# Optimization experiments

Hardware: AMD Instinct MI355X
Metric: run time of the kernel (lower is better)

## Reference

```python
import jax, jax.numpy as jnp
import numpy as np


def setup_inputs() -> dict:
    key = jax.random.key(0)
    k1, k2, k3, k4, k5 = jax.random.split(key, 5)
    B, D, T = 32, 256, 32       # batch, word_feature_dim, seq_len
    Dh, H, Wd = 128, 128, 128   # image_feature_dim, height, width
    word_features = jax.random.normal(k1, (B, D, T), dtype=jnp.float32)
    image_features = jax.random.normal(k2, (B, Dh, H, Wd), dtype=jnp.float32)
    words_mask = jax.random.randint(k3, (B, T), 0, 2, dtype=jnp.int32)
    W = jax.random.normal(k4, (Dh, D), dtype=jnp.float32) * (1.0 / np.sqrt(D))
    b = jax.random.normal(k5, (Dh,), dtype=jnp.float32) * 0.01
    return {"word_features": word_features, "image_features": image_features,
            "words_mask": words_mask, "W": W, "b": b}


def reference(word_features, image_features, words_mask, W, b):
    B, D, T = word_features.shape
    Dh = image_features.shape[1]
    N = image_features.shape[2] * image_features.shape[3]  # H*W
    # values = fc(word_features^T)^T : [B, Dh, T]
    values = jnp.einsum('bdt,kd->bkt', word_features, W) + b[None, :, None]
    # queries: [B, N, Dh] (flatten spatial)
    queries = image_features.reshape(B, Dh, N)
    # scores S: [B, N, T]
    S = jnp.einsum('bkn,bkt->bnt', queries, values)
    mask = (words_mask != 0)[:, None, :]  # [B,1,T], True => masked
    S = jnp.where(mask, -jnp.inf, S)
    # softmax over seq dim (original: exp / sum(exp)); stable form is same math
    attn_coefficients = jax.nn.softmax(S, axis=2)  # [B, N, T]
    # context vectors: [B, Dh, N]
    attn = jnp.einsum('bkt,bnt->bkn', values, attn_coefficients)
    return attn, attn_coefficients
```

## Files before the change

kernel.cpp:

```cpp
#include <hip/hip_runtime.h>
#include <math.h>

constexpr int Bc  = 32;
constexpr int Dc  = 256;
constexpr int Tc  = 32;
constexpr int DHc = 128;
constexpr int Nc  = 16384;

typedef _Float16 v8hf __attribute__((ext_vector_type(8)));
typedef _Float16 v2hf __attribute__((ext_vector_type(2)));
typedef float    v4f  __attribute__((ext_vector_type(4)));

__global__ __launch_bounds__(256) void values_kernel(
    const float* __restrict__ wf, const float* __restrict__ Wm,
    const float* __restrict__ bias,
    _Float16* __restrict__ vth, _Float16* __restrict__ vtl,
    _Float16* __restrict__ vph)
{
    __shared__ float wfs[Dc * Tc];
    __shared__ float Ws[16 * 260];

    const int tid = threadIdx.x;
    const int b   = blockIdx.x >> 3;
    const int k0  = (blockIdx.x & 7) * 16;

    {
        const float4* src = (const float4*)(wf + (size_t)b * Dc * Tc);
        float4* dst = (float4*)wfs;
        #pragma unroll
        for (int i = 0; i < 8; ++i) dst[tid + 256 * i] = src[tid + 256 * i];
    }
    {
        #pragma unroll
        for (int i = 0; i < 4; ++i) {
            int f = tid + 256 * i;
            int row = f >> 6, d4 = f & 63;
            *(float4*)&Ws[row * 260 + 4 * d4] =
                *(const float4*)&Wm[(size_t)(k0 + row) * Dc + 4 * d4];
        }
    }
    __syncthreads();

    const int kl  = tid >> 4;
    const int tt0 = (tid & 15) * 2;
    const int k   = k0 + kl;

    float acc0 = bias[k], acc1 = acc0;
    #pragma unroll
    for (int d4 = 0; d4 < 64; ++d4) {
        const float4 w4 = *(const float4*)&Ws[kl * 260 + 4 * d4];
        #pragma unroll
        for (int j = 0; j < 4; ++j) {
            const float2 f2 = *(const float2*)&wfs[(4 * d4 + j) * Tc + tt0];
            const float wv = (j == 0) ? w4.x : (j == 1) ? w4.y : (j == 2) ? w4.z : w4.w;
            acc0 = fmaf(wv, f2.x, acc0);
            acc1 = fmaf(wv, f2.y, acc1);
        }
    }

    _Float16 vh0 = (_Float16)acc0, vh1 = (_Float16)acc1;
    _Float16 vl0 = (_Float16)(acc0 - (float)vh0);
    _Float16 vl1 = (_Float16)(acc1 - (float)vh1);

    {
        v2hf p; p[0] = vh0; p[1] = vh1;
        *(v2hf*)&vph[((size_t)b * DHc + k) * Tc + tt0] = p;
    }
    vth[((size_t)b * Tc + tt0)     * DHc + k] = vh0;
    vth[((size_t)b * Tc + tt0 + 1) * DHc + k] = vh1;
    vtl[((size_t)b * Tc + tt0)     * DHc + k] = vl0;
    vtl[((size_t)b * Tc + tt0 + 1) * DHc + k] = vl1;
}

__device__ __forceinline__ _Float16 pick_half(int u, int sel) {
    unsigned short s = (unsigned short)(sel ? (u >> 16) : u);
    return __builtin_bit_cast(_Float16, s);
}

__global__ __launch_bounds__(256) void attn_kernel(
    const float* __restrict__ img,
    const _Float16* __restrict__ vth, const _Float16* __restrict__ vtl,
    const _Float16* __restrict__ vph,
    const int* __restrict__ mask, float* __restrict__ attn,
    float* __restrict__ coeff)
{
    constexpr int VT_LD = 136;
    constexpr int VP_LD = 40;
    __shared__ __align__(16) _Float16 VTh[Tc * VT_LD];
    __shared__ __align__(16) _Float16 VTl[Tc * VT_LD];
    __shared__ __align__(16) _Float16 VPh[DHc * VP_LD];
    __shared__ float mneg[Tc];

    const int tid   = threadIdx.x;
    const int b     = blockIdx.x >> 7;
    const int strip = blockIdx.x & 127;

    {
        const uint4* sth = (const uint4*)(vth + (size_t)b * Tc * DHc);
        const uint4* stl = (const uint4*)(vtl + (size_t)b * Tc * DHc);
        const uint4* sph = (const uint4*)(vph + (size_t)b * DHc * Tc);
        #pragma unroll
        for (int i = 0; i < 2; ++i) {
            int cid = tid + 256 * i;
            int t = cid >> 4, cc = cid & 15;
            *(uint4*)&VTh[t * VT_LD + 8 * cc] = sth[cid];
            *(uint4*)&VTl[t * VT_LD + 8 * cc] = stl[cid];
            int kk = cid >> 2, c4 = cid & 3;
            *(uint4*)&VPh[kk * VP_LD + 8 * c4] = sph[cid];
        }
        if (tid < Tc) mneg[tid] = mask[b * Tc + tid] ? -INFINITY : 0.0f;
    }
    __syncthreads();

    const int lane = tid & 63;
    const int wave = tid >> 6;
    const int c    = lane & 15;
    const int g    = lane >> 4;

    float madd[2][4];
    #pragma unroll
    for (int tt = 0; tt < 2; ++tt)
        #pragma unroll
        for (int r = 0; r < 4; ++r)
            madd[tt][r] = mneg[16 * tt + 4 * g + r];

    const float* qbase = img  + ((size_t)b * DHc + 8 * g) * Nc + c;
    float*       abase = attn + ((size_t)b * DHc + c) * Nc + 4 * g;
    float*       cbase = coeff + (size_t)b * Nc * Tc;

    const int ls_lo = c + 32 * (g & 1);
    const int sel   = g >> 1;

    #pragma unroll
    for (int it = 0; it < 2; ++it) {
        const int n0 = strip * 128 + (it * 4 + wave) * 16;

        const float* qp = qbase + n0;
        v8hf Qh[4], Ql[4];
        #pragma unroll
        for (int ks = 0; ks < 4; ++ks)
            #pragma unroll
            for (int j = 0; j < 8; ++j) {
                float qv = qp[(size_t)(ks * 32 + j) * Nc];
                _Float16 h = (_Float16)qv;
                Qh[ks][j] = h;
                Ql[ks][j] = (_Float16)(qv - (float)h);
            }

        v4f Sh[2], Sl[2];
        #pragma unroll
        for (int tt = 0; tt < 2; ++tt) {
            Sh[tt] = (v4f){0.f, 0.f, 0.f, 0.f};
            Sl[tt] = (v4f){0.f, 0.f, 0.f, 0.f};
        }
        #pragma unroll
        for (int tt = 0; tt < 2; ++tt) {
            const int rowbase = (16 * tt + c) * VT_LD + 8 * g;
            #pragma unroll
            for (int ks = 0; ks < 4; ++ks) {
                v8hf va = *(const v8hf*)&VTh[rowbase + ks * 32];
                v8hf vl = *(const v8hf*)&VTl[rowbase + ks * 32];
                Sh[tt] = __builtin_amdgcn_mfma_f32_16x16x32_f16(va, Qh[ks], Sh[tt], 0, 0, 0);
                Sl[tt] = __builtin_amdgcn_mfma_f32_16x16x32_f16(va, Ql[ks], Sl[tt], 0, 0, 0);
                Sl[tt] = __builtin_amdgcn_mfma_f32_16x16x32_f16(vl, Qh[ks], Sl[tt], 0, 0, 0);
            }
        }

        float p0[4], p1[4];
        float m = -INFINITY;
        #pragma unroll
        for (int r = 0; r < 4; ++r) {
            p0[r] = Sh[0][r] + Sl[0][r] + madd[0][r];
            p1[r] = Sh[1][r] + Sl[1][r] + madd[1][r];
            m = fmaxf(m, fmaxf(p0[r], p1[r]));
        }
        m = fmaxf(m, __shfl_xor(m, 16));
        m = fmaxf(m, __shfl_xor(m, 32));
        float sum = 0.0f;
        #pragma unroll
        for (int r = 0; r < 4; ++r) {
            p0[r] = __expf(p0[r] - m); sum += p0[r];
            p1[r] = __expf(p1[r] - m); sum += p1[r];
        }
        sum += __shfl_xor(sum, 16);
        sum += __shfl_xor(sum, 32);
        const float inv = 1.0f / sum;
        #pragma unroll
        for (int r = 0; r < 4; ++r) { p0[r] *= inv; p1[r] *= inv; }

        float* cp = cbase + (size_t)(n0 + c) * Tc + 4 * g;
        *(float4*)cp        = make_float4(p0[0], p0[1], p0[2], p0[3]);
        *(float4*)(cp + 16) = make_float4(p1[0], p1[1], p1[2], p1[3]);

        v8hf Pb;
        #pragma unroll
        for (int r = 0; r < 4; ++r) {
            v2hf h2; h2[0] = (_Float16)p0[r]; h2[1] = (_Float16)p1[r];
            int u   = __builtin_bit_cast(int, h2);
            int ulo = __shfl(u, ls_lo);
            int uhi = __shfl(u, ls_lo + 16);
            Pb[r]     = pick_half(ulo, sel);
            Pb[4 + r] = pick_half(uhi, sel);
        }

        #pragma unroll
        for (int mt = 0; mt < 8; ++mt) {
            v8hf vb2 = *(const v8hf*)&VPh[(16 * mt + c) * VP_LD + 8 * g];
            v4f o = (v4f){0.f, 0.f, 0.f, 0.f};
            o = __builtin_amdgcn_mfma_f32_16x16x32_f16(Pb, vb2, o, 0, 0, 0);
            float* ap = abase + (size_t)(16 * mt) * Nc + n0;
            *(float4*)ap = make_float4(o[0], o[1], o[2], o[3]);
        }
    }
}

extern "C" void kernel_launch(void* const* d_in, const int* in_sizes, int n_in,
                              void* d_out, int out_size, void* d_ws, size_t ws_size,
                              hipStream_t stream)
{
    const float* wf   = (const float*)d_in[0];
    const float* img  = (const float*)d_in[1];
    const int*   msk  = (const int*)d_in[2];
    const float* Wm   = (const float*)d_in[3];
    const float* bias = (const float*)d_in[4];

    float* attn  = (float*)d_out;
    float* coeff = attn + (size_t)Bc * DHc * Nc;

    _Float16* vth = (_Float16*)d_ws;
    _Float16* vtl = vth + (size_t)Bc * DHc * Tc;
    _Float16* vph = vtl + (size_t)Bc * DHc * Tc;

    values_kernel<<<256, 256, 0, stream>>>(wf, Wm, bias, vth, vtl, vph);
    attn_kernel<<<Bc * 128, 256, 0, stream>>>(img, vth, vtl, vph, msk, attn, coeff);
}
```

Measured before the change: 538.8 us.

## Stage values writes through LDS, use nontemporal output stores, raise MFMA priority

```diff
diff --git a/kernel.cpp b/kernel.cpp
--- a/kernel.cpp
+++ b/kernel.cpp
@@ -62,19 +62,42 @@
     _Float16 vl0 = (_Float16)(acc0 - (float)vh0);
     _Float16 vl1 = (_Float16)(acc1 - (float)vh1);
 
-    {
-        v2hf p; p[0] = vh0; p[1] = vh1;
-        *(v2hf*)&vph[((size_t)b * DHc + k) * Tc + tt0] = p;
-    }
-    vth[((size_t)b * Tc + tt0)     * DHc + k] = vh0;
-    vth[((size_t)b * Tc + tt0 + 1) * DHc + k] = vh1;
-    vtl[((size_t)b * Tc + tt0)     * DHc + k] = vl0;
-    vtl[((size_t)b * Tc + tt0 + 1) * DHc + k] = vl1;
+    __syncthreads();
+    _Float16* sh_h = (_Float16*)wfs;
+    _Float16* th_h = sh_h + 16 * 32;
+    _Float16* th_l = th_h + 32 * 24;
+
+    sh_h[kl * 32 + tt0]     = vh0;
+    sh_h[kl * 32 + tt0 + 1] = vh1;
+    th_h[tt0 * 24 + kl]       = vh0;
+    th_h[(tt0 + 1) * 24 + kl] = vh1;
+    th_l[tt0 * 24 + kl]       = vl0;
+    th_l[(tt0 + 1) * 24 + kl] = vl1;
+    __syncthreads();
+
+    if (tid < 64) {
+        int row = tid >> 2, ch = (tid & 3) * 8;
+        *(uint4*)&vph[((size_t)b * DHc + k0 + row) * Tc + ch] =
+            *(uint4*)&sh_h[row * 32 + ch];
+    } else if (tid < 128) {
+        int i = tid - 64; int t = i >> 1, hf = (i & 1) * 8;
+        *(uint4*)&vth[((size_t)b * Tc + t) * DHc + k0 + hf] =
+            *(uint4*)&th_h[t * 24 + hf];
+    } else if (tid < 192) {
+        int i = tid - 128; int t = i >> 1, hf = (i & 1) * 8;
+        *(uint4*)&vtl[((size_t)b * Tc + t) * DHc + k0 + hf] =
+            *(uint4*)&th_l[t * 24 + hf];
+    }
 }
 
 __device__ __forceinline__ _Float16 pick_half(int u, int sel) {
     unsigned short s = (unsigned short)(sel ? (u >> 16) : u);
     return __builtin_bit_cast(_Float16, s);
+}
+
+__device__ __forceinline__ void nt_store4(float* p, float a, float b2, float c, float d) {
+    v4f v; v[0] = a; v[1] = b2; v[2] = c; v[3] = d;
+    __builtin_nontemporal_store(v, (v4f*)p);
 }
 
 __global__ __launch_bounds__(256) void attn_kernel(
@@ -153,6 +176,7 @@
             Sh[tt] = (v4f){0.f, 0.f, 0.f, 0.f};
             Sl[tt] = (v4f){0.f, 0.f, 0.f, 0.f};
         }
+        __builtin_amdgcn_s_setprio(1);
         #pragma unroll
         for (int tt = 0; tt < 2; ++tt) {
             const int rowbase = (16 * tt + c) * VT_LD + 8 * g;
@@ -165,6 +189,7 @@
                 Sl[tt] = __builtin_amdgcn_mfma_f32_16x16x32_f16(vl, Qh[ks], Sl[tt], 0, 0, 0);
             }
         }
+        __builtin_amdgcn_s_setprio(0);
 
         float p0[4], p1[4];
         float m = -INFINITY;
@@ -189,8 +214,8 @@
         for (int r = 0; r < 4; ++r) { p0[r] *= inv; p1[r] *= inv; }
 
         float* cp = cbase + (size_t)(n0 + c) * Tc + 4 * g;
-        *(float4*)cp        = make_float4(p0[0], p0[1], p0[2], p0[3]);
-        *(float4*)(cp + 16) = make_float4(p1[0], p1[1], p1[2], p1[3]);
+        nt_store4(cp,      p0[0], p0[1], p0[2], p0[3]);
+        nt_store4(cp + 16, p1[0], p1[1], p1[2], p1[3]);
 
         v8hf Pb;
         #pragma unroll
@@ -203,14 +228,16 @@
             Pb[4 + r] = pick_half(uhi, sel);
         }
 
+        __builtin_amdgcn_s_setprio(1);
         #pragma unroll
         for (int mt = 0; mt < 8; ++mt) {
             v8hf vb2 = *(const v8hf*)&VPh[(16 * mt + c) * VP_LD + 8 * g];
             v4f o = (v4f){0.f, 0.f, 0.f, 0.f};
             o = __builtin_amdgcn_mfma_f32_16x16x32_f16(Pb, vb2, o, 0, 0, 0);
             float* ap = abase + (size_t)(16 * mt) * Nc + n0;
-            *(float4*)ap = make_float4(o[0], o[1], o[2], o[3]);
-        }
+            nt_store4(ap, o[0], o[1], o[2], o[3]);
+        }
+        __builtin_amdgcn_s_setprio(0);
     }
 }
 
```

Result: slower. 555.2 us (+3.0%).
